# Performance work log

Hardware: AMD Instinct MI355X
Metric: run time of the kernel (lower is better)

## Reference

```python
import jax, jax.numpy as jnp
import numpy as np


def setup_inputs() -> dict:
    key = jax.random.key(0)
    ks = jax.random.split(key, 6)
    B, Lq, Lm, D = 4, 2048, 2048, 1024
    s = D ** -0.5
    return {
        "input": jax.random.normal(ks[0], (B, Lq, D), jnp.float32),
        "memory": jax.random.normal(ks[1], (B, Lm, D), jnp.float32),
        # torch Linear weights are [out_features, in_features]
        "Wq": jax.random.normal(ks[2], (D, D), jnp.float32) * s,
        "Wk": jax.random.normal(ks[3], (D, D), jnp.float32) * s,
        "Wv": jax.random.normal(ks[4], (D, D), jnp.float32) * s,
        "Wo": jax.random.normal(ks[5], (D, D), jnp.float32) * s,
    }


def reference(input, memory, Wq, Wk, Wv, Wo):
    # q/k/v projections (Linear, no bias): x @ W.T
    depth = Wq.shape[0]
    q = jnp.einsum("bqd,ed->bqe", input, Wq) * (depth ** -0.5)
    k = jnp.einsum("bmd,ed->bme", memory, Wk)
    v = jnp.einsum("bmd,ed->bme", memory, Wv)
    logit = jnp.einsum("bqe,bme->bqm", q, k)          # [B, Lq, Lm]
    attention_weight = jax.nn.softmax(logit, axis=-1)
    attention_output = jnp.einsum("bqm,bme->bqe", attention_weight, v)
    return jnp.einsum("bqe,oe->bqo", attention_output, Wo)
```

## Files before the change

### kernel.cpp

```cpp
#include <hip/hip_runtime.h>
#include <hip/hip_bf16.h>

typedef unsigned short u16;
typedef __bf16 bf16x8 __attribute__((ext_vector_type(8)));
typedef float floatx4 __attribute__((ext_vector_type(4)));
typedef __hip_bfloat16 bf;

__device__ __forceinline__ __bf16 f2b(float f) {
    __hip_bfloat16 h = __float2bfloat16(f);
    return *reinterpret_cast<__bf16*>(&h);
}
__device__ __forceinline__ bf16x8 ld8f(const float* p) {
    float4 a = ((const float4*)p)[0];
    float4 b = ((const float4*)p)[1];
    bf16x8 r;
    r[0] = f2b(a.x); r[1] = f2b(a.y); r[2] = f2b(a.z); r[3] = f2b(a.w);
    r[4] = f2b(b.x); r[5] = f2b(b.y); r[6] = f2b(b.z); r[7] = f2b(b.w);
    return r;
}
__device__ __forceinline__ void storev(float* p, float v) { *p = v; }
__device__ __forceinline__ void storev(bf* p, float v)    { *p = __float2bfloat16(v); }

__device__ __forceinline__ void gl16(const bf* g, u16* l) {
    __builtin_amdgcn_global_load_lds(
        (const __attribute__((address_space(1))) void*)g,
        (__attribute__((address_space(3))) void*)l, 16, 0, 0);
}


#define FENCE asm volatile("" ::: "memory")
#define BARx  __builtin_amdgcn_s_barrier()
#define LGKM0 asm volatile("s_waitcnt lgkmcnt(0)" ::: "memory")
#define VM3   asm volatile("s_waitcnt vmcnt(3)" ::: "memory")
#define VM0   asm volatile("s_waitcnt vmcnt(0)" ::: "memory")

#define ST_A(h, kt, Ab) \
    gl16(Asrc + (long)((h) * 32) * K + (long)(kt) * 64, (Ab) + (h) * 4096 + tid * 8)
#define ST_Bu0(c, kt, Bb) \
    gl16(Bsrc + (long)((c) * 32) * K + (long)(kt) * 64, (Bb) + (c) * 8192 + tid * 8)
#define ST_Bu1(c, kt, Bb) \
    gl16(Bsrc + (long)((c) * 32 + 128) * K + (long)(kt) * 64, (Bb) + (c) * 8192 + 4096 + tid * 8)

#define RD_A(dst, h, Ab) do { _Pragma("unroll") \
    for (int q_ = 0; q_ < 2; q_++) { \
        const u16* p_ = (Ab) + ((h) * 64 + wg * 32 + q_ * 16 + fr) * 64; \
        dst[q_ * 2 + 0] = *(const bf16x8*)(p_ + kl0); \
        dst[q_ * 2 + 1] = *(const bf16x8*)(p_ + kl1); \
    } } while (0)

#define RD_B(dst, c, Bb) do { _Pragma("unroll") \
    for (int j_ = 0; j_ < 2; j_++) { \
        const u16* p_ = (Bb) + ((c) * 128 + w4 * 32 + j_ * 16 + fr) * 64; \
        dst[j_ * 2 + 0] = *(const bf16x8*)(p_ + kl0); \
        dst[j_ * 2 + 1] = *(const bf16x8*)(p_ + kl1); \
    } } while (0)

#define QMM(h, c, av, bv) do { _Pragma("unroll") \
    for (int q_ = 0; q_ < 2; q_++) _Pragma("unroll") \
    for (int j_ = 0; j_ < 2; j_++) _Pragma("unroll") \
    for (int kk_ = 0; kk_ < 2; kk_++) \
        acc[(h) * 2 + q_][(c) * 2 + j_] = __builtin_amdgcn_mfma_f32_16x16x32_bf16( \
            av[q_ * 2 + kk_], bv[j_ * 2 + kk_], acc[(h) * 2 + q_][(c) * 2 + j_], 0, 0, 0); \
} while (0)

template <typename OutT>
__device__ __forceinline__ void gemm8_core(
    const bf* __restrict__ A, const bf* __restrict__ B, OutT* __restrict__ C,
    int K, int N, int m_blk, int n_blk, float scale, u16* lds)
{
    const int tid  = threadIdx.x;
    const int w    = tid >> 6, lane = tid & 63;
    const int wg   = w >> 2, w4 = w & 3;
    const int fr   = lane & 15, kg = lane >> 4;

    u16* const A0b = lds;
    u16* const B0b = lds + 8192;
    u16* const A1b = lds + 24576;
    u16* const B1b = lds + 32768;

    const int kl0 = (kg * 8) ^ ((fr & 7) << 3);
    const int kl1 = kl0 ^ 32;

    const int sr  = tid >> 3;
    const int scs = ((tid & 7) * 8) ^ ((sr & 7) << 3);
    const bf* Asrc = A + (long)(m_blk + (tid >> 8) * 64 + (sr & 31)) * K + scs;
    const bf* Bsrc = B + (long)(n_blk + (tid >> 8) * 64 + (sr & 31)) * K + scs;

    floatx4 acc[4][4];
#pragma unroll
    for (int i = 0; i < 4; i++)
#pragma unroll
        for (int j = 0; j < 4; j++) acc[i][j] = (floatx4){0.f, 0.f, 0.f, 0.f};

    bf16x8 a0[4], a1[4], b0[4], b1[4];

    const int T     = K >> 6;
    const int iters = T >> 1;

    ST_A(0, 0, A0b); ST_A(1, 0, A0b);
    ST_Bu0(0, 0, B0b); ST_Bu1(0, 0, B0b); ST_Bu0(1, 0, B0b); ST_Bu1(1, 0, B0b);
    ST_A(0, 1, A1b); ST_A(1, 1, A1b);
    ST_Bu0(0, 1, B1b); ST_Bu1(0, 1, B1b); ST_Bu0(1, 1, B1b); ST_Bu1(1, 1, B1b);
    VM0; BARx;

    for (int it = 0; it < iters; ++it) {
        const int t   = it * 2;
        const int ts0 = (t + 2 < T) ? t + 2 : 0;
        const int ts1 = (t + 3 < T) ? t + 3 : 0;

        RD_A(a0, 0, A0b); RD_A(a1, 1, A0b); RD_B(b0, 0, B0b);
        if (it) { ST_Bu1(0, t + 1, B1b); ST_Bu0(1, t + 1, B1b); ST_Bu1(1, t + 1, B1b); }
        FENCE; BARx; LGKM0;
        __builtin_amdgcn_s_setprio(1); QMM(0, 0, a0, b0); QMM(1, 0, a1, b0);
        __builtin_amdgcn_s_setprio(0); FENCE; BARx;

        RD_B(b1, 1, B0b);
        ST_A(0, ts0, A0b); ST_A(1, ts0, A0b); ST_Bu0(0, ts0, B0b);
        FENCE; BARx; LGKM0;
        __builtin_amdgcn_s_setprio(1); QMM(0, 1, a0, b1); QMM(1, 1, a1, b1);
        __builtin_amdgcn_s_setprio(0); VM3; FENCE; BARx;

        RD_A(a0, 0, A1b); RD_A(a1, 1, A1b); RD_B(b0, 0, B1b);
        ST_Bu1(0, ts0, B0b); ST_Bu0(1, ts0, B0b); ST_Bu1(1, ts0, B0b);
        FENCE; BARx; LGKM0;
        __builtin_amdgcn_s_setprio(1); QMM(0, 0, a0, b0); QMM(1, 0, a1, b0);
        __builtin_amdgcn_s_setprio(0); FENCE; BARx;

        RD_B(b1, 1, B1b);
        ST_A(0, ts1, A1b); ST_A(1, ts1, A1b); ST_Bu0(0, ts1, B1b);
        FENCE; BARx; LGKM0;
        __builtin_amdgcn_s_setprio(1); QMM(0, 1, a0, b1); QMM(1, 1, a1, b1);
        __builtin_amdgcn_s_setprio(0); VM3; FENCE; BARx;
    }

    const long c_col0 = n_blk + w4 * 64 + fr;
    const long c_row0 = m_blk + wg * 64 + (lane >> 4) * 4;
#pragma unroll
    for (int rf = 0; rf < 4; rf++)
#pragma unroll
        for (int r = 0; r < 4; r++) {
            const long row = c_row0 + rf * 16 + r;
#pragma unroll
            for (int cf = 0; cf < 4; cf++)
                storev(&C[row * N + c_col0 + cf * 16], acc[rf][cf][r] * scale);
        }
}

template <typename OutT>
__global__ __launch_bounds__(512)
void gemm8(const bf* __restrict__ A, const bf* __restrict__ B,
           OutT* __restrict__ C, int K, int N,
           long sA, long sB, long sC, float scale)
{
    __shared__ __align__(16) u16 lds[49152];
    gemm8_core(A + blockIdx.z * sA, B + blockIdx.z * sB, C + blockIdx.z * sC,
               K, N, blockIdx.y * 128, blockIdx.x * 256, scale, lds);
}

__global__ __launch_bounds__(512)
void gemm8_qk(const bf* __restrict__ xb, const bf* __restrict__ memb,
              const bf* __restrict__ Wqb, const bf* __restrict__ Wkb,
              bf* __restrict__ Q, bf* __restrict__ Kp, float qscale)
{
    __shared__ __align__(16) u16 lds[49152];
    const int z = blockIdx.z;
    gemm8_core(z ? memb : xb, z ? Wkb : Wqb, z ? Kp : Q, 1024, 1024,
               blockIdx.y * 128, blockIdx.x * 256, z ? 1.f : qscale, lds);
}

__global__ __launch_bounds__(256)
void cvt2(const float* __restrict__ a, const float* __restrict__ b,
          bf* __restrict__ da, bf* __restrict__ db, long n)
{
    const float* s = blockIdx.z ? b : a;
    bf* d = blockIdx.z ? db : da;
    const long stride = (long)gridDim.x * 256;
    for (long i = (long)blockIdx.x * 256 + threadIdx.x; i * 8 < n; i += stride)
        *(bf16x8*)(d + i * 8) = ld8f(s + i * 8);
}

__global__ __launch_bounds__(256)
void cvt_w(const float* __restrict__ w0, const float* __restrict__ w1,
           const float* __restrict__ w2, const float* __restrict__ w3,
           bf* __restrict__ d)
{
    const int z = blockIdx.z;
    const float* s = (z == 0) ? w0 : (z == 1) ? w1 : (z == 2) ? w2 : w3;
    bf* dz = d + (long)z * (1 << 20);
    const long i = ((long)blockIdx.x * 256 + threadIdx.x) * 8;
    *(bf16x8*)(dz + i) = ld8f(s + i);
}

__global__ __launch_bounds__(256)
void softmax_rows_2048(bf* __restrict__ X)
{
    const long row = blockIdx.x;
    const int t = threadIdx.x;
    const int wave = t >> 6, lane = t & 63;
    __shared__ float red[8];

    float v[8];
    float m = -1e30f;
#pragma unroll
    for (int i = 0; i < 8; i++) {
        v[i] = __bfloat162float(X[row * 2048 + t + i * 256]);
        m = fmaxf(m, v[i]);
    }
#pragma unroll
    for (int o = 32; o > 0; o >>= 1) m = fmaxf(m, __shfl_xor(m, o, 64));
    if (lane == 0) red[wave] = m;
    __syncthreads();
    m = fmaxf(fmaxf(red[0], red[1]), fmaxf(red[2], red[3]));

    float s = 0.f;
#pragma unroll
    for (int i = 0; i < 8; i++) { v[i] = __expf(v[i] - m); s += v[i]; }
#pragma unroll
    for (int o = 32; o > 0; o >>= 1) s += __shfl_xor(s, o, 64);
    if (lane == 0) red[4 + wave] = s;
    __syncthreads();
    s = red[4] + red[5] + red[6] + red[7];

    const float inv = 1.f / s;
#pragma unroll
    for (int i = 0; i < 8; i++)
        X[row * 2048 + t + i * 256] = __float2bfloat16(v[i] * inv);
}

extern "C" void kernel_launch(void* const* d_in, const int* in_sizes, int n_in,
                              void* d_out, int out_size, void* d_ws, size_t ws_size,
                              hipStream_t stream)
{
    const float* x   = (const float*)d_in[0];
    const float* mem = (const float*)d_in[1];
    const float* Wq  = (const float*)d_in[2];
    const float* Wk  = (const float*)d_in[3];
    const float* Wv  = (const float*)d_in[4];
    const float* Wo  = (const float*)d_in[5];

    constexpr int  B = 4, L = 2048, D = 1024;
    constexpr long LD = (long)L * D;
    constexpr long LL = (long)L * L;
    constexpr size_t CH = 1u << 24;

    char* ws = (char*)d_ws;
    bf* Q   = (bf*)(ws + 0 * CH);
    bf* Kp  = (bf*)(ws + 1 * CH);
    bf* Vt  = (bf*)(ws + 2 * CH);
    bf* Wb  = (bf*)(ws + 3 * CH);
    bf* Wqb = Wb;
    bf* Wkb = Wb + (long)(1 << 20);
    bf* Wvb = Wb + (long)2 * (1 << 20);
    bf* Wob = Wb + (long)3 * (1 << 20);
    bf* AO  = Q;

    bf* xb   = (bf*)d_out;
    bf* memb = (bf*)d_out + B * LD;
    bf* Lg   = (bf*)d_out;

    const float qscale = 0.03125f;

    cvt2<<<dim3(1024, 1, 2), dim3(256), 0, stream>>>(x, mem, xb, memb, B * LD);
    cvt_w<<<dim3(512, 1, 4), dim3(256), 0, stream>>>(Wq, Wk, Wv, Wo, Wb);

    gemm8_qk<<<dim3(4, 64, 2), dim3(512), 0, stream>>>(
        xb, memb, Wqb, Wkb, Q, Kp, qscale);

    gemm8<bf><<<dim3(8, 8, 4), dim3(512), 0, stream>>>(
        Wvb, memb, Vt, D, L, 0, LD, (long)D * L, 1.f);

    gemm8<bf><<<dim3(8, 16, 4), dim3(512), 0, stream>>>(
        Q, Kp, Lg, D, L, LD, LD, LL, 1.f);

    softmax_rows_2048<<<dim3(B * L), dim3(256), 0, stream>>>(Lg);

    gemm8<bf><<<dim3(4, 16, 4), dim3(512), 0, stream>>>(
        Lg, Vt, AO, L, D, LL, (long)D * L, LD, 1.f);

    gemm8<float><<<dim3(4, 64, 1), dim3(512), 0, stream>>>(
        AO, Wob, (float*)d_out, D, D, 0, 0, 0, 1.f);
}
```

Before: 300.4 us.

## Add 256x256-tile GEMM kernel and XCD-aware block swizzle for large GEMMs

Adds a new 256x256 output-tile GEMM core with double-buffered 128KB LDS and a reworked load/compute interleave. It is used for the QK projection and the QK^T logits GEMMs. It also adds a block-index swizzle that groups consecutive block IDs so neighbouring tiles land on the same XCD, which should improve L2 reuse, and applies it to the existing 128x256 kernels. The larger tile raises arithmetic intensity per LDS load but halves the block count and raises register and LDS pressure, which could limit occupancy and leave CUs idle on the smaller grids.

```diff
diff --git a/kernel.cpp b/kernel.cpp
--- a/kernel.cpp
+++ b/kernel.cpp
@@ -27,12 +27,180 @@
         (__attribute__((address_space(3))) void*)l, 16, 0, 0);
 }
 
+__device__ __forceinline__ void swz3(int& bx, int& by, int& bz) {
+    const int nx = gridDim.x, ny = gridDim.y, nz = gridDim.z;
+    const int lid = blockIdx.x + nx * (blockIdx.y + ny * blockIdx.z);
+    const int cpx = (nx * ny * nz) >> 3;
+    const int s = (lid & 7) * cpx + (lid >> 3);
+    bx = s % nx;
+    const int r = s / nx;
+    by = r % ny;
+    bz = r / ny;
+}
 
 #define FENCE asm volatile("" ::: "memory")
 #define BARx  __builtin_amdgcn_s_barrier()
 #define LGKM0 asm volatile("s_waitcnt lgkmcnt(0)" ::: "memory")
 #define VM3   asm volatile("s_waitcnt vmcnt(3)" ::: "memory")
+#define VM6   asm volatile("s_waitcnt vmcnt(6)" ::: "memory")
 #define VM0   asm volatile("s_waitcnt vmcnt(0)" ::: "memory")
+
+
+#define ST_A2(u, kt, Ab) \
+    gl16(Asrc + (long)((u) * 64) * K + (long)(kt) * 64, (Ab) + (u) * 4096 + tid * 8)
+#define ST_B2(u, kt, Bb) \
+    gl16(Bsrc + (long)((u) * 64) * K + (long)(kt) * 64, (Bb) + (u) * 4096 + tid * 8)
+
+#define RD_A2(dst, h, Ab) do { _Pragma("unroll") \
+    for (int q_ = 0; q_ < 4; q_++) { \
+        const u16* p_ = (Ab) + (wg * 128 + (h) * 64 + q_ * 16 + fr) * 64; \
+        dst[q_ * 2 + 0] = *(const bf16x8*)(p_ + kl0); \
+        dst[q_ * 2 + 1] = *(const bf16x8*)(p_ + kl1); \
+    } } while (0)
+
+#define RD_B2(dst, c, Bb) do { _Pragma("unroll") \
+    for (int j_ = 0; j_ < 2; j_++) { \
+        const u16* p_ = (Bb) + (w4 * 64 + (c) * 32 + j_ * 16 + fr) * 64; \
+        dst[j_ * 2 + 0] = *(const bf16x8*)(p_ + kl0); \
+        dst[j_ * 2 + 1] = *(const bf16x8*)(p_ + kl1); \
+    } } while (0)
+
+#define QMM2(h, c, av, bv) do { _Pragma("unroll") \
+    for (int q_ = 0; q_ < 4; q_++) _Pragma("unroll") \
+    for (int j_ = 0; j_ < 2; j_++) _Pragma("unroll") \
+    for (int kk_ = 0; kk_ < 2; kk_++) \
+        acc[(h) * 4 + q_][(c) * 2 + j_] = __builtin_amdgcn_mfma_f32_16x16x32_bf16( \
+            av[q_ * 2 + kk_], bv[j_ * 2 + kk_], acc[(h) * 4 + q_][(c) * 2 + j_], 0, 0, 0); \
+} while (0)
+
+template <typename OutT>
+__device__ __forceinline__ void gemm256_core(
+    const bf* __restrict__ A, const bf* __restrict__ B, OutT* __restrict__ C,
+    int K, int N, int m_blk, int n_blk, float scale, u16* lds)
+{
+    const int tid = threadIdx.x;
+    const int w = tid >> 6, lane = tid & 63;
+    const int wg = w >> 2, w4 = w & 3;
+    const int fr = lane & 15, kg = lane >> 4;
+
+    u16* const A0b = lds;
+    u16* const B0b = lds + 16384;
+    u16* const A1b = lds + 32768;
+    u16* const B1b = lds + 49152;
+
+    const int kl0 = (kg * 8) ^ ((fr & 7) << 3);
+    const int kl1 = kl0 ^ 32;
+
+    const int sr  = tid >> 3;
+    const int scs = ((tid & 7) * 8) ^ ((sr & 7) << 3);
+    const bf* Asrc = A + (long)(m_blk + sr) * K + scs;
+    const bf* Bsrc = B + (long)(n_blk + sr) * K + scs;
+
+    floatx4 acc[8][4];
+#pragma unroll
+    for (int i = 0; i < 8; i++)
+#pragma unroll
+        for (int j = 0; j < 4; j++) acc[i][j] = (floatx4){0.f, 0.f, 0.f, 0.f};
+
+    bf16x8 a[8], b0[4], b1[4];
+
+    const int T     = K >> 6;
+    const int iters = T >> 1;
+
+#pragma unroll
+    for (int u = 0; u < 4; u++) { ST_A2(u, 0, A0b); ST_B2(u, 0, B0b); }
+#pragma unroll
+    for (int u = 0; u < 4; u++) { ST_A2(u, 1, A1b); ST_B2(u, 1, B1b); }
+    VM0; BARx;
+
+    for (int it = 0; it < iters; ++it) {
+        const int t   = it * 2;
+        const int ts0 = (t + 2 < T) ? t + 2 : 0;
+        const int ts1 = (t + 3 < T) ? t + 3 : 0;
+
+        RD_A2(a, 0, A0b); RD_B2(b0, 0, B0b);
+        if (it) { ST_A2(1, t + 1, A1b); ST_A2(3, t + 1, A1b); }
+        FENCE; BARx; LGKM0;
+        __builtin_amdgcn_s_setprio(1); QMM2(0, 0, a, b0);
+        __builtin_amdgcn_s_setprio(0); FENCE; BARx;
+
+        RD_B2(b1, 1, B0b);
+        ST_A2(0, ts0, A0b); ST_A2(2, ts0, A0b);
+        FENCE; BARx; LGKM0;
+        __builtin_amdgcn_s_setprio(1); QMM2(0, 1, a, b1);
+        __builtin_amdgcn_s_setprio(0); FENCE; BARx;
+
+        RD_A2(a, 1, A0b);
+        ST_B2(0, ts0, B0b); ST_B2(1, ts0, B0b);
+        FENCE; BARx; LGKM0;
+        __builtin_amdgcn_s_setprio(1); QMM2(1, 1, a, b1);
+        __builtin_amdgcn_s_setprio(0); FENCE; BARx;
+
+        ST_B2(2, ts0, B0b); ST_B2(3, ts0, B0b);
+        FENCE; BARx;
+        __builtin_amdgcn_s_setprio(1); QMM2(1, 0, a, b0);
+        __builtin_amdgcn_s_setprio(0); VM6; FENCE; BARx;
+
+        RD_A2(a, 0, A1b); RD_B2(b0, 0, B1b);
+        ST_A2(1, ts0, A0b); ST_A2(3, ts0, A0b);
+        FENCE; BARx; LGKM0;
+        __builtin_amdgcn_s_setprio(1); QMM2(0, 0, a, b0);
+        __builtin_amdgcn_s_setprio(0); FENCE; BARx;
+
+        RD_B2(b1, 1, B1b);
+        ST_A2(0, ts1, A1b); ST_A2(2, ts1, A1b);
+        FENCE; BARx; LGKM0;
+        __builtin_amdgcn_s_setprio(1); QMM2(0, 1, a, b1);
+        __builtin_amdgcn_s_setprio(0); FENCE; BARx;
+
+        RD_A2(a, 1, A1b);
+        ST_B2(0, ts1, B1b); ST_B2(1, ts1, B1b);
+        FENCE; BARx; LGKM0;
+        __builtin_amdgcn_s_setprio(1); QMM2(1, 1, a, b1);
+        __builtin_amdgcn_s_setprio(0); FENCE; BARx;
+
+        ST_B2(2, ts1, B1b); ST_B2(3, ts1, B1b);
+        FENCE; BARx;
+        __builtin_amdgcn_s_setprio(1); QMM2(1, 0, a, b0);
+        __builtin_amdgcn_s_setprio(0); VM6; FENCE; BARx;
+    }
+
+    const long c_col0 = n_blk + w4 * 64 + fr;
+    const long c_row0 = m_blk + wg * 128 + (lane >> 4) * 4;
+#pragma unroll
+    for (int rf = 0; rf < 8; rf++)
+#pragma unroll
+        for (int r = 0; r < 4; r++) {
+            const long row = c_row0 + rf * 16 + r;
+#pragma unroll
+            for (int cf = 0; cf < 4; cf++)
+                storev(&C[row * N + c_col0 + cf * 16], acc[rf][cf][r] * scale);
+        }
+}
+
+template <typename OutT>
+__global__ __launch_bounds__(512)
+void gemm256(const bf* __restrict__ A, const bf* __restrict__ B,
+             OutT* __restrict__ C, int K, int N,
+             long sA, long sB, long sC, float scale)
+{
+    __shared__ __align__(16) u16 lds[65536];
+    int bx, by, bz; swz3(bx, by, bz);
+    gemm256_core(A + bz * sA, B + bz * sB, C + bz * sC,
+                 K, N, by * 256, bx * 256, scale, lds);
+}
+
+__global__ __launch_bounds__(512)
+void gemm256_qk(const bf* __restrict__ xb, const bf* __restrict__ memb,
+                const bf* __restrict__ Wqb, const bf* __restrict__ Wkb,
+                bf* __restrict__ Q, bf* __restrict__ Kp, float qscale)
+{
+    __shared__ __align__(16) u16 lds[65536];
+    int bx, by, bz; swz3(bx, by, bz);
+    gemm256_core(bz ? memb : xb, bz ? Wkb : Wqb, bz ? Kp : Q, 1024, 1024,
+                 by * 256, bx * 256, bz ? 1.f : qscale, lds);
+}
+
 
 #define ST_A(h, kt, Ab) \
     gl16(Asrc + (long)((h) * 32) * K + (long)(kt) * 64, (Ab) + (h) * 4096 + tid * 8)
@@ -64,7 +232,7 @@
 } while (0)
 
 template <typename OutT>
-__device__ __forceinline__ void gemm8_core(
+__device__ __forceinline__ void gemm128_core(
     const bf* __restrict__ A, const bf* __restrict__ B, OutT* __restrict__ C,
     int K, int N, int m_blk, int n_blk, float scale, u16* lds)
 {
@@ -148,24 +316,14 @@
 
 template <typename OutT>
 __global__ __launch_bounds__(512)
-void gemm8(const bf* __restrict__ A, const bf* __restrict__ B,
-           OutT* __restrict__ C, int K, int N,
-           long sA, long sB, long sC, float scale)
+void gemm128(const bf* __restrict__ A, const bf* __restrict__ B,
+             OutT* __restrict__ C, int K, int N,
+             long sA, long sB, long sC, float scale)
 {
     __shared__ __align__(16) u16 lds[49152];
-    gemm8_core(A + blockIdx.z * sA, B + blockIdx.z * sB, C + blockIdx.z * sC,
-               K, N, blockIdx.y * 128, blockIdx.x * 256, scale, lds);
-}
-
-__global__ __launch_bounds__(512)
-void gemm8_qk(const bf* __restrict__ xb, const bf* __restrict__ memb,
-              const bf* __restrict__ Wqb, const bf* __restrict__ Wkb,
-              bf* __restrict__ Q, bf* __restrict__ Kp, float qscale)
-{
-    __shared__ __align__(16) u16 lds[49152];
-    const int z = blockIdx.z;
-    gemm8_core(z ? memb : xb, z ? Wkb : Wqb, z ? Kp : Q, 1024, 1024,
-               blockIdx.y * 128, blockIdx.x * 256, z ? 1.f : qscale, lds);
+    int bx, by, bz; swz3(bx, by, bz);
+    gemm128_core(A + bz * sA, B + bz * sB, C + bz * sC,
+                 K, N, by * 128, bx * 256, scale, lds);
 }
 
 __global__ __launch_bounds__(256)
@@ -263,20 +421,20 @@
     cvt2<<<dim3(1024, 1, 2), dim3(256), 0, stream>>>(x, mem, xb, memb, B * LD);
     cvt_w<<<dim3(512, 1, 4), dim3(256), 0, stream>>>(Wq, Wk, Wv, Wo, Wb);
 
-    gemm8_qk<<<dim3(4, 64, 2), dim3(512), 0, stream>>>(
+    gemm256_qk<<<dim3(4, 32, 2), dim3(512), 0, stream>>>(
         xb, memb, Wqb, Wkb, Q, Kp, qscale);
 
-    gemm8<bf><<<dim3(8, 8, 4), dim3(512), 0, stream>>>(
+    gemm128<bf><<<dim3(8, 8, 4), dim3(512), 0, stream>>>(
         Wvb, memb, Vt, D, L, 0, LD, (long)D * L, 1.f);
 
-    gemm8<bf><<<dim3(8, 16, 4), dim3(512), 0, stream>>>(
+    gemm256<bf><<<dim3(8, 8, 4), dim3(512), 0, stream>>>(
         Q, Kp, Lg, D, L, LD, LD, LL, 1.f);
 
     softmax_rows_2048<<<dim3(B * L), dim3(256), 0, stream>>>(Lg);
 
-    gemm8<bf><<<dim3(4, 16, 4), dim3(512), 0, stream>>>(
+    gemm128<bf><<<dim3(4, 16, 4), dim3(512), 0, stream>>>(
         Lg, Vt, AO, L, D, LL, (long)D * L, LD, 1.f);
 
-    gemm8<float><<<dim3(4, 64, 1), dim3(512), 0, stream>>>(
+    gemm128<float><<<dim3(4, 64, 1), dim3(512), 0, stream>>>(
         AO, Wob, (float*)d_out, D, D, 0, 0, 0, 1.f);
 }
```

After: 296.9 us. About the same (-1.2%).

## Software-pipeline GEMM MFMA one stage behind LDS reads and swizzle block order

Applied to the files above, without the earlier changes.

Restructures the GEMM main loop so each phase's MFMAs run on fragments loaded in the previous phase, overlapping LDS reads and global-to-LDS stores with matrix math. It also removes one barrier per phase and double-buffers the register fragments. Separately, it remaps the block index so consecutive workgroups are spread across the 8 XCDs (swz3), aiming at better L2 locality. Risks are higher register pressure, from doubling the fragment registers, and subtle LDS hazards in the reordered barriers.

```diff
diff --git a/kernel.cpp b/kernel.cpp
--- a/kernel.cpp
+++ b/kernel.cpp
@@ -27,12 +27,25 @@
         (__attribute__((address_space(3))) void*)l, 16, 0, 0);
 }
 
+__device__ __forceinline__ void swz3(int& bx, int& by, int& bz) {
+    const int nx = gridDim.x, ny = gridDim.y, nz = gridDim.z;
+    const int lid = blockIdx.x + nx * (blockIdx.y + ny * blockIdx.z);
+    const int cpx = (nx * ny * nz) >> 3;
+    const int s = (lid & 7) * cpx + (lid >> 3);
+    bx = s % nx;
+    const int r = s / nx;
+    by = r % ny;
+    bz = r / ny;
+}
 
 #define FENCE asm volatile("" ::: "memory")
 #define BARx  __builtin_amdgcn_s_barrier()
 #define LGKM0 asm volatile("s_waitcnt lgkmcnt(0)" ::: "memory")
 #define VM3   asm volatile("s_waitcnt vmcnt(3)" ::: "memory")
 #define VM0   asm volatile("s_waitcnt vmcnt(0)" ::: "memory")
+#define SP1   __builtin_amdgcn_s_setprio(1)
+#define SP0   __builtin_amdgcn_s_setprio(0)
+
 
 #define ST_A(h, kt, Ab) \
     gl16(Asrc + (long)((h) * 32) * K + (long)(kt) * 64, (Ab) + (h) * 4096 + tid * 8)
@@ -55,16 +68,18 @@
         dst[j_ * 2 + 1] = *(const bf16x8*)(p_ + kl1); \
     } } while (0)
 
-#define QMM(h, c, av, bv) do { _Pragma("unroll") \
+#define MBLK(c, a0v, a1v, bv) do { _Pragma("unroll") \
     for (int q_ = 0; q_ < 2; q_++) _Pragma("unroll") \
     for (int j_ = 0; j_ < 2; j_++) _Pragma("unroll") \
-    for (int kk_ = 0; kk_ < 2; kk_++) \
-        acc[(h) * 2 + q_][(c) * 2 + j_] = __builtin_amdgcn_mfma_f32_16x16x32_bf16( \
-            av[q_ * 2 + kk_], bv[j_ * 2 + kk_], acc[(h) * 2 + q_][(c) * 2 + j_], 0, 0, 0); \
-} while (0)
+    for (int kk_ = 0; kk_ < 2; kk_++) { \
+        acc[q_][(c) * 2 + j_] = __builtin_amdgcn_mfma_f32_16x16x32_bf16( \
+            a0v[q_ * 2 + kk_], bv[j_ * 2 + kk_], acc[q_][(c) * 2 + j_], 0, 0, 0); \
+        acc[2 + q_][(c) * 2 + j_] = __builtin_amdgcn_mfma_f32_16x16x32_bf16( \
+            a1v[q_ * 2 + kk_], bv[j_ * 2 + kk_], acc[2 + q_][(c) * 2 + j_], 0, 0, 0); \
+    } } while (0)
 
 template <typename OutT>
-__device__ __forceinline__ void gemm8_core(
+__device__ __forceinline__ void gemm128_core(
     const bf* __restrict__ A, const bf* __restrict__ B, OutT* __restrict__ C,
     int K, int N, int m_blk, int n_blk, float scale, u16* lds)
 {
@@ -92,7 +107,8 @@
 #pragma unroll
         for (int j = 0; j < 4; j++) acc[i][j] = (floatx4){0.f, 0.f, 0.f, 0.f};
 
-    bf16x8 a0[4], a1[4], b0[4], b1[4];
+    bf16x8 aX0[4], aX1[4], aY0[4], aY1[4];
+    bf16x8 b0X[4], b1X[4], b0Y[4], b1Y[4];
 
     const int T     = K >> 6;
     const int iters = T >> 1;
@@ -101,37 +117,36 @@
     ST_Bu0(0, 0, B0b); ST_Bu1(0, 0, B0b); ST_Bu0(1, 0, B0b); ST_Bu1(1, 0, B0b);
     ST_A(0, 1, A1b); ST_A(1, 1, A1b);
     ST_Bu0(0, 1, B1b); ST_Bu1(0, 1, B1b); ST_Bu0(1, 1, B1b); ST_Bu1(1, 1, B1b);
-    VM0; BARx;
+    VM0; BARx; FENCE;
 
     for (int it = 0; it < iters; ++it) {
         const int t   = it * 2;
         const int ts0 = (t + 2 < T) ? t + 2 : 0;
         const int ts1 = (t + 3 < T) ? t + 3 : 0;
 
-        RD_A(a0, 0, A0b); RD_A(a1, 1, A0b); RD_B(b0, 0, B0b);
-        if (it) { ST_Bu1(0, t + 1, B1b); ST_Bu0(1, t + 1, B1b); ST_Bu1(1, t + 1, B1b); }
-        FENCE; BARx; LGKM0;
-        __builtin_amdgcn_s_setprio(1); QMM(0, 0, a0, b0); QMM(1, 0, a1, b0);
-        __builtin_amdgcn_s_setprio(0); FENCE; BARx;
-
-        RD_B(b1, 1, B0b);
+        RD_A(aX0, 0, A0b); RD_A(aX1, 1, A0b); RD_B(b0X, 0, B0b);
+        if (it) {
+            ST_Bu1(0, t + 1, B1b); ST_Bu0(1, t + 1, B1b); ST_Bu1(1, t + 1, B1b);
+            SP1; MBLK(1, aY0, aY1, b1Y); SP0;
+        }
+        LGKM0; BARx; FENCE;
+
+        RD_B(b1X, 1, B0b);
         ST_A(0, ts0, A0b); ST_A(1, ts0, A0b); ST_Bu0(0, ts0, B0b);
-        FENCE; BARx; LGKM0;
-        __builtin_amdgcn_s_setprio(1); QMM(0, 1, a0, b1); QMM(1, 1, a1, b1);
-        __builtin_amdgcn_s_setprio(0); VM3; FENCE; BARx;
-
-        RD_A(a0, 0, A1b); RD_A(a1, 1, A1b); RD_B(b0, 0, B1b);
+        SP1; MBLK(0, aX0, aX1, b0X); SP0;
+        LGKM0; VM3; BARx; FENCE;
+
+        RD_A(aY0, 0, A1b); RD_A(aY1, 1, A1b); RD_B(b0Y, 0, B1b);
         ST_Bu1(0, ts0, B0b); ST_Bu0(1, ts0, B0b); ST_Bu1(1, ts0, B0b);
-        FENCE; BARx; LGKM0;
-        __builtin_amdgcn_s_setprio(1); QMM(0, 0, a0, b0); QMM(1, 0, a1, b0);
-        __builtin_amdgcn_s_setprio(0); FENCE; BARx;
-
-        RD_B(b1, 1, B1b);
+        SP1; MBLK(1, aX0, aX1, b1X); SP0;
+        LGKM0; BARx; FENCE;
+
+        RD_B(b1Y, 1, B1b);
         ST_A(0, ts1, A1b); ST_A(1, ts1, A1b); ST_Bu0(0, ts1, B1b);
-        FENCE; BARx; LGKM0;
-        __builtin_amdgcn_s_setprio(1); QMM(0, 1, a0, b1); QMM(1, 1, a1, b1);
-        __builtin_amdgcn_s_setprio(0); VM3; FENCE; BARx;
+        SP1; MBLK(0, aY0, aY1, b0Y); SP0;
+        LGKM0; VM3; BARx; FENCE;
     }
+    MBLK(1, aY0, aY1, b1Y);
 
     const long c_col0 = n_blk + w4 * 64 + fr;
     const long c_row0 = m_blk + wg * 64 + (lane >> 4) * 4;
@@ -148,24 +163,25 @@
 
 template <typename OutT>
 __global__ __launch_bounds__(512)
-void gemm8(const bf* __restrict__ A, const bf* __restrict__ B,
-           OutT* __restrict__ C, int K, int N,
-           long sA, long sB, long sC, float scale)
+void gemm128(const bf* __restrict__ A, const bf* __restrict__ B,
+             OutT* __restrict__ C, int K, int N,
+             long sA, long sB, long sC, float scale)
 {
     __shared__ __align__(16) u16 lds[49152];
-    gemm8_core(A + blockIdx.z * sA, B + blockIdx.z * sB, C + blockIdx.z * sC,
-               K, N, blockIdx.y * 128, blockIdx.x * 256, scale, lds);
+    int bx, by, bz; swz3(bx, by, bz);
+    gemm128_core(A + bz * sA, B + bz * sB, C + bz * sC,
+                 K, N, by * 128, bx * 256, scale, lds);
 }
 
 __global__ __launch_bounds__(512)
-void gemm8_qk(const bf* __restrict__ xb, const bf* __restrict__ memb,
-              const bf* __restrict__ Wqb, const bf* __restrict__ Wkb,
-              bf* __restrict__ Q, bf* __restrict__ Kp, float qscale)
+void gemm128_qk(const bf* __restrict__ xb, const bf* __restrict__ memb,
+                const bf* __restrict__ Wqb, const bf* __restrict__ Wkb,
+                bf* __restrict__ Q, bf* __restrict__ Kp, float qscale)
 {
     __shared__ __align__(16) u16 lds[49152];
-    const int z = blockIdx.z;
-    gemm8_core(z ? memb : xb, z ? Wkb : Wqb, z ? Kp : Q, 1024, 1024,
-               blockIdx.y * 128, blockIdx.x * 256, z ? 1.f : qscale, lds);
+    int bx, by, bz; swz3(bx, by, bz);
+    gemm128_core(bz ? memb : xb, bz ? Wkb : Wqb, bz ? Kp : Q, 1024, 1024,
+                 by * 128, bx * 256, bz ? 1.f : qscale, lds);
 }
 
 __global__ __launch_bounds__(256)
@@ -263,20 +279,20 @@
     cvt2<<<dim3(1024, 1, 2), dim3(256), 0, stream>>>(x, mem, xb, memb, B * LD);
     cvt_w<<<dim3(512, 1, 4), dim3(256), 0, stream>>>(Wq, Wk, Wv, Wo, Wb);
 
-    gemm8_qk<<<dim3(4, 64, 2), dim3(512), 0, stream>>>(
+    gemm128_qk<<<dim3(4, 64, 2), dim3(512), 0, stream>>>(
         xb, memb, Wqb, Wkb, Q, Kp, qscale);
 
-    gemm8<bf><<<dim3(8, 8, 4), dim3(512), 0, stream>>>(
+    gemm128<bf><<<dim3(8, 8, 4), dim3(512), 0, stream>>>(
         Wvb, memb, Vt, D, L, 0, LD, (long)D * L, 1.f);
 
-    gemm8<bf><<<dim3(8, 16, 4), dim3(512), 0, stream>>>(
+    gemm128<bf><<<dim3(8, 16, 4), dim3(512), 0, stream>>>(
         Q, Kp, Lg, D, L, LD, LD, LL, 1.f);
 
     softmax_rows_2048<<<dim3(B * L), dim3(256), 0, stream>>>(Lg);
 
-    gemm8<bf><<<dim3(4, 16, 4), dim3(512), 0, stream>>>(
+    gemm128<bf><<<dim3(4, 16, 4), dim3(512), 0, stream>>>(
         Lg, Vt, AO, L, D, LL, (long)D * L, LD, 1.f);
 
-    gemm8<float><<<dim3(4, 64, 1), dim3(512), 0, stream>>>(
+    gemm128<float><<<dim3(4, 64, 1), dim3(512), 0, stream>>>(
         AO, Wob, (float*)d_out, D, D, 0, 0, 0, 1.f);
 }
```

Result: faster. 294.3 us (-2.0%).
